# Optimization experiments

Measured on AMD Instinct MI355X. Metric: run time of the kernel, lower is better.

## Reference

```python
import jax, jax.numpy as jnp
import numpy as np

D_MODEL = 1024
D_STATE = 16
EPS = 1e-5


def _layernorm(x, g, b):
    mu = x.mean(-1, keepdims=True)
    xc = x - mu
    var = (xc * xc).mean(-1, keepdims=True)
    return xc * jax.lax.rsqrt(var + EPS) * g + b


def setup_inputs() -> dict:
    key = jax.random.key(0)
    ks = jax.random.split(key, 10)
    B, L, d, n = 8, 1024, D_MODEL, D_STATE
    s = 1.0 / np.sqrt(d)
    return {
        "x": jax.random.normal(ks[0], (B, L, d), jnp.float32),
        "h_prev": jnp.zeros((B, d * n), jnp.float32),
        "ln_g": jnp.ones((d,), jnp.float32),
        "ln_b": jnp.zeros((d,), jnp.float32),
        "W_ig": jax.random.uniform(ks[1], (2 * d, d), jnp.float32, -s, s),
        "W_dt": jax.random.uniform(ks[2], (d, d), jnp.float32, -s, s),
        "b_dt": jax.random.uniform(ks[3], (d,), jnp.float32, -s, s),
        "A_log": jax.random.uniform(ks[4], (d, n), jnp.float32, -3.0, -1.0),
        "W_B": jax.random.uniform(ks[5], (n, d), jnp.float32, -s, s),
        "W_C": jax.random.uniform(ks[6], (n, d), jnp.float32, -s, s),
        "D": jnp.ones((d,), jnp.float32),
        "W_out": jax.random.uniform(ks[7], (d, d), jnp.float32, -s, s),
    }


def reference(x, h_prev, ln_g, ln_b, W_ig, W_dt, b_dt, A_log, W_B, W_C, D, W_out):
    Bsz, L, d = x.shape
    n = A_log.shape[1]
    x_norm = _layernorm(x, ln_g, ln_b)
    x_proj = jnp.einsum('bld,ed->ble', x_norm, W_ig)  # [B,L,2d]
    x_in, z = x_proj[..., :d], x_proj[..., d:]
    dt = jax.nn.softplus(jnp.einsum('bld,ed->ble', x_in, W_dt) + b_dt)  # [B,L,d]
    A = -jnp.exp(A_log)  # [d,n]
    B_t = jnp.einsum('bld,nd->bln', x_in, W_B)  # [B,L,n]
    C_t = jnp.einsum('bld,nd->bln', x_in, W_C)  # [B,L,n]
    h0 = h_prev.reshape(Bsz, d, n)

    def step(h, inp):
        dt_t, xin_t, Bt_t, Ct_t = inp  # [B,d],[B,d],[B,n],[B,n]
        dA = jnp.exp(dt_t[..., None] * A)                      # [B,d,n]
        h = dA * h + (dt_t * xin_t)[..., None] * Bt_t[:, None, :]
        y_t = (h * Ct_t[:, None, :]).sum(-1)                   # [B,d]
        return h, y_t

    xs = (jnp.swapaxes(dt, 0, 1), jnp.swapaxes(x_in, 0, 1),
          jnp.swapaxes(B_t, 0, 1), jnp.swapaxes(C_t, 0, 1))
    h_final, y = jax.lax.scan(step, h0, xs)
    y = jnp.swapaxes(y, 0, 1)  # [B,L,d]
    ssm_out = y * jax.nn.silu(z) + x_in * D
    out = jnp.einsum('bld,ed->ble', ssm_out, W_out)
    return (x + out, h_final.reshape(Bsz, -1))
```

## Files before the change

kernel.cpp:

```cpp
#include <hip/hip_runtime.h>
#include <hip/hip_bf16.h>
#include <math.h>

#define DM 1024
#define NS 16
#define BSZ 8
#define LSEQ 1024
#define MROWS (BSZ*LSEQ)
#define CH 32
#define ROWP 36
#define YSP 18

typedef __bf16 bf16;
typedef bf16 bf16x8 __attribute__((ext_vector_type(8)));
typedef bf16 bf16x4 __attribute__((ext_vector_type(4)));
typedef float f32x4 __attribute__((ext_vector_type(4)));
typedef float f32x2 __attribute__((ext_vector_type(2)));
typedef unsigned int u32;
typedef unsigned short u16;
typedef u32 u32x4 __attribute__((ext_vector_type(4)));

__device__ __forceinline__ void async16(const void* g, void* l) {
  __builtin_amdgcn_global_load_lds((const __attribute__((address_space(1))) void*)g,
                                   (__attribute__((address_space(3))) void*)l,
                                   16, 0, 0);
}

__device__ __forceinline__ float bflo(u32 u) { return __builtin_bit_cast(float, (u32)(u << 16)); }
__device__ __forceinline__ float bfhi(u32 u) { return __builtin_bit_cast(float, (u32)(u & 0xffff0000u)); }

__global__ __launch_bounds__(256)
void preproc(const float* __restrict__ W_ig, const float* __restrict__ W_dt,
             const float* __restrict__ W_B, const float* __restrict__ W_C,
             const float* __restrict__ W_out,
             bf16* __restrict__ wmega, bf16* __restrict__ wstack,
             bf16* __restrict__ wout, bf16* __restrict__ wigT,
             const float* __restrict__ x, const float* __restrict__ ln_g,
             const float* __restrict__ ln_b, bf16* __restrict__ xnorm) {
  __shared__ float tile[64][65];
  const int blk = blockIdx.x;
  const int t = threadIdx.x;

  if (blk < 4128) {
    int i = blk * 256 + t;
    const float* s; bf16* d; int base;
    if (i < 524288)      { s = W_ig;  d = wmega;                           base = 0; }
    else if (i < 786432) { s = W_dt;  d = wstack;                          base = 524288; }
    else if (i < 790528) { s = W_B;   d = wstack + (size_t)DM * DM;        base = 786432; }
    else if (i < 794624) { s = W_C;   d = wstack + (size_t)(DM + NS) * DM; base = 790528; }
    else                 { s = W_out; d = wout;                            base = 794624; }
    int k = i - base;
    float4 v = ((const float4*)s)[k];
    bf16x4 o;
    o.x = (bf16)v.x; o.y = (bf16)v.y; o.z = (bf16)v.z; o.w = (bf16)v.w;
    *(bf16x4*)(d + 4 * (size_t)k) = o;
  } else if (blk < 4384) {
    int tb = blk - 4128;
    const int bk = (tb & 15) * 64;
    const int bd = (tb >> 4) * 64;
    const int c4 = t & 15;
    const int r0 = t >> 4;
#pragma unroll
    for (int p = 0; p < 4; ++p) {
      int r = r0 + p * 16;
      float4 v = *(const float4*)(W_ig + (size_t)(bd + r) * 1024 + bk + c4 * 4);
      tile[r][c4 * 4 + 0] = v.x;
      tile[r][c4 * 4 + 1] = v.y;
      tile[r][c4 * 4 + 2] = v.z;
      tile[r][c4 * 4 + 3] = v.w;
    }
    __syncthreads();
#pragma unroll
    for (int p = 0; p < 4; ++p) {
      int r = r0 + p * 16;
      bf16x4 o;
      o.x = (bf16)tile[c4 * 4 + 0][r];
      o.y = (bf16)tile[c4 * 4 + 1][r];
      o.z = (bf16)tile[c4 * 4 + 2][r];
      o.w = (bf16)tile[c4 * 4 + 3][r];
      *(bf16x4*)(wigT + (size_t)(bk + r) * 1024 + bd + c4 * 4) = o;
    }
  } else {
    const size_t row = blk - 4384;
    float4 v = ((const float4*)(x + row * DM))[t];
    float s = v.x + v.y + v.z + v.w;
    float s2 = v.x*v.x + v.y*v.y + v.z*v.z + v.w*v.w;
#pragma unroll
    for (int m = 1; m < 64; m <<= 1) { s += __shfl_xor(s, m, 64); s2 += __shfl_xor(s2, m, 64); }
    __shared__ float red[8];
    int wave = t >> 6, lane = t & 63;
    if (lane == 0) { red[wave] = s; red[4 + wave] = s2; }
    __syncthreads();
    s  = red[0] + red[1] + red[2] + red[3];
    s2 = red[4] + red[5] + red[6] + red[7];
    float mu  = s * (1.f / DM);
    float var = s2 * (1.f / DM) - mu * mu;
    float inv = rsqrtf(var + 1e-5f);
    float4 gg = ((const float4*)ln_g)[t];
    float4 bb = ((const float4*)ln_b)[t];
    bf16x4 o;
    o.x = (bf16)((v.x - mu) * inv * gg.x + bb.x);
    o.y = (bf16)((v.y - mu) * inv * gg.y + bb.y);
    o.z = (bf16)((v.z - mu) * inv * gg.z + bb.z);
    o.w = (bf16)((v.w - mu) * inv * gg.w + bb.w);
    *(bf16x4*)(xnorm + row * DM + t * 4) = o;
  }
}

template <int EPI, bool SWZ>
__global__ __launch_bounds__(256)
void gemm_bf16(const bf16* __restrict__ A, const bf16* __restrict__ W, int K,
               float* __restrict__ out_f, bf16* __restrict__ out_b,
               u16* __restrict__ out_u1, u16* __restrict__ out_u2,
               const float* __restrict__ aux,
               float* __restrict__ out_f3, float* __restrict__ out_f4) {
  __shared__ bf16 As[3][128 * 32];
  __shared__ bf16 Bs[3][128 * 32];
  int tx, ty;
  if (SWZ) {
    int g = blockIdx.x;
    int xcd = g & 7, slot = g >> 3;
    tx = slot >> 3;
    ty = xcd * 8 + (slot & 7);
  } else {
    tx = blockIdx.x; ty = blockIdx.y;
  }
  const int tid  = threadIdx.x;
  const int wave = tid >> 6, lane = tid & 63;
  const int lr = lane & 15, quad = lane >> 4;
  const size_t arow = (size_t)ty * 128;
  const size_t brow = (size_t)tx * 128;
  f32x4 acc[4][4] = {};

  const int srl  = lane >> 2;
  const int kg   = lane & 3;
  const int srow = wave * 32 + srl;
  const int skc  = (kg ^ ((srl >> 1) & 3)) * 8;
  const bf16* ag = A + (arow + srow) * (size_t)K + skc;
  const bf16* wg = W + (brow + srow) * (size_t)K + skc;

  const int soff = wave * 32 * 32;
  const int ra   = (((wave >> 1) * 64) + lr) * 32 + ((quad ^ ((lr >> 1) & 3)) * 8);
  const int rb   = (((wave & 1)  * 64) + lr) * 32 + ((quad ^ ((lr >> 1) & 3)) * 8);

  bf16 *aw0 = &As[0][soff], *aw1 = &As[1][soff], *aw2 = &As[2][soff];
  bf16 *bw0 = &Bs[0][soff], *bw1 = &Bs[1][soff], *bw2 = &Bs[2][soff];
  const bf16 *ar0 = &As[0][ra], *ar1 = &As[1][ra], *ar2 = &As[2][ra];
  const bf16 *br0 = &Bs[0][rb], *br1 = &Bs[1][rb], *br2 = &Bs[2][rb];

  auto STAGE = [&](bf16* adst, bf16* bdst, int kk) {
    async16(ag + kk,                       adst);
    async16(ag + (size_t)16 * K + kk,      adst + 16 * 32);
    async16(wg + kk,                       bdst);
    async16(wg + (size_t)16 * K + kk,      bdst + 16 * 32);
  };
  auto COMPUTE = [&](const bf16* ap, const bf16* bp) {
    bf16x8 af[4], bfr[4];
#pragma unroll
    for (int i = 0; i < 4; ++i) af[i] = *(const bf16x8*)(ap + i * 16 * 32);
#pragma unroll
    for (int j = 0; j < 4; ++j) bfr[j] = *(const bf16x8*)(bp + j * 16 * 32);
#pragma unroll
    for (int i = 0; i < 4; ++i)
#pragma unroll
      for (int j = 0; j < 4; ++j)
        acc[i][j] = __builtin_amdgcn_mfma_f32_16x16x32_bf16(af[i], bfr[j], acc[i][j], 0, 0, 0);
  };

  STAGE(aw0, bw0, 0);
  STAGE(aw1, bw1, 32);
  asm volatile("s_waitcnt vmcnt(4)" ::: "memory");
  __builtin_amdgcn_s_barrier();

  for (int k0 = 0; k0 < K; k0 += 32) {
    const bool pf = (k0 + 64 < K);
    if (pf) STAGE(aw2, bw2, k0 + 64);
    COMPUTE(ar0, br0);
    if (pf) asm volatile("s_waitcnt vmcnt(4)" ::: "memory");
    else    asm volatile("s_waitcnt vmcnt(0)" ::: "memory");
    __builtin_amdgcn_s_barrier();
    bf16* t0;
    t0 = aw0; aw0 = aw1; aw1 = aw2; aw2 = t0;
    t0 = bw0; bw0 = bw1; bw1 = bw2; bw2 = t0;
    const bf16* t1;
    t1 = ar0; ar0 = ar1; ar1 = ar2; ar2 = t1;
    t1 = br0; br0 = br1; br1 = br2; br2 = t1;
  }

  const size_t mbase = arow + (wave >> 1) * 64;
  const size_t nbase = brow + (wave & 1) * 64;
  if (EPI == 0) {
    if (nbase < 3 * DM) {
      u16* dst; size_t gbase; bool is_dt = false;
      if (nbase < DM)            { dst = out_u1;       gbase = nbase >> 4; }
      else if (nbase < 2 * DM)   { dst = (u16*)out_b;  gbase = (nbase - DM) >> 4; }
      else                       { dst = out_u2;       gbase = (nbase - 2 * DM) >> 4; is_dt = true; }
      bf16* lds_ep = &As[0][0] + (size_t)wave * 1024;
#pragma unroll
      for (int j = 0; j < 4; ++j) {
#pragma unroll
        for (int i = 0; i < 4; ++i)
#pragma unroll
          for (int r = 0; r < 4; ++r) {
            float v = acc[i][j][r];
            if (is_dt) {
              float tt = v + aux[nbase - 2 * DM + j * 16 + lr];
              v = (tt > 20.f) ? tt : __logf(1.f + __expf(tt));
            }
            lds_ep[(i * 16 + quad * 4 + r) * 16 + lr] = (bf16)v;
          }
        u32x4 v0 = *(u32x4*)&lds_ep[lane * 16];
        u32x4 v1 = *(u32x4*)&lds_ep[lane * 16 + 8];
        size_t off = ((gbase + j) * (size_t)MROWS + mbase + lane) * 16;
        *(u32x4*)&dst[off]     = v0;
        *(u32x4*)&dst[off + 8] = v1;
      }
    } else if (nbase < 3 * DM + 2 * NS) {
#pragma unroll
      for (int i = 0; i < 4; ++i)
#pragma unroll
        for (int r = 0; r < 4; ++r) {
          size_t m = mbase + i * 16 + quad * 4 + r;
          out_f3[m * NS + lr] = acc[i][0][r];
          out_f4[m * NS + lr] = acc[i][1][r];
        }
    }
  } else {
#pragma unroll
    for (int i = 0; i < 4; ++i)
#pragma unroll
      for (int j = 0; j < 4; ++j)
#pragma unroll
        for (int r = 0; r < 4; ++r) {
          size_t m = mbase + i * 16 + quad * 4 + r;
          size_t n = nbase + j * 16 + lr;
          float v = acc[i][j][r];
          if (EPI == 2) {
            out_f[m * DM + n] = v + aux[m * DM + n];
          } else {
            out_b[m * (size_t)DM + n] = (bf16)v;
          }
        }
  }
}

__global__ __launch_bounds__(256)
void scan_kernel(const u16* __restrict__ dt_b, const u16* __restrict__ xi_b,
                 const bf16* __restrict__ z_b,
                 const float* __restrict__ B_t, const float* __restrict__ C_t,
                 const float* __restrict__ A_log, const float* __restrict__ h_prev,
                 const float* __restrict__ Dvec,
                 bf16* __restrict__ ssm_out, float* __restrict__ h_final) {
  const int blk = blockIdx.x;
  const int b = blk >> 6;
  const int g = blk & 63;
  const int d0 = g * 16;
  const int t = threadIdx.x;
  const int n = t & 15, dl = t >> 4;
  const int d = d0 + dl;
  const float Ac2 = -__expf(A_log[d * NS + n]) * 1.44269504f;
  float h = h_prev[(size_t)b * DM * NS + (size_t)d * NS + n];

  __shared__ u32   dxs[2][16][ROWP];
  __shared__ float Bsh[2][16][ROWP];
  __shared__ float Csh[2][16][ROWP];
  __shared__ float ys_p[CH][16][YSP];

  const size_t base_row = (size_t)b * LSEQ;
  const size_t base16 = ((size_t)g * MROWS + base_row) * 16;
  const int pl = t >> 3, pc = (2 * t) & 15;
  const int l_a = t >> 4, c_a = t & 15;
  const float Dva = Dvec[d0 + c_a];

  {
    u32 D = ((const u32*)(dt_b + base16))[t];
    u32 X = ((const u32*)(xi_b + base16))[t];
    dxs[0][pc][pl]     = (D & 0xffffu) | (X << 16);
    dxs[0][pc + 1][pl] = (D >> 16) | (X & 0xffff0000u);
    size_t gB = base_row * NS;
    f32x2 B2 = ((const f32x2*)(B_t + gB))[t];
    f32x2 C2 = ((const f32x2*)(C_t + gB))[t];
    Bsh[0][pc][pl] = B2.x;  Bsh[0][pc + 1][pl] = B2.y;
    Csh[0][pc][pl] = C2.x;  Csh[0][pc + 1][pl] = C2.y;
  }
  float za = (float)z_b[base16 + t];
  float zb = (float)z_b[base16 + 256 + t];
  __syncthreads();

  for (int c = 0; c < LSEQ / CH; ++c) {
    const int cur = c & 1, nxt = cur ^ 1;
    u32 pD, pX; f32x2 pB2, pC2; float pza, pzb;
    if (c + 1 < LSEQ / CH) {
      size_t off = base16 + (size_t)(c + 1) * (CH * 16);
      pD = ((const u32*)(dt_b + off))[t];
      pX = ((const u32*)(xi_b + off))[t];
      pza = (float)z_b[off + t]; pzb = (float)z_b[off + 256 + t];
      size_t gB = (base_row + (size_t)(c + 1) * CH) * NS;
      pB2 = ((const f32x2*)(B_t + gB))[t];
      pC2 = ((const f32x2*)(C_t + gB))[t];
    }
#pragma unroll
    for (int l4 = 0; l4 < CH; l4 += 4) {
      u32x4 dx4 = *(const u32x4*)&dxs[cur][dl][l4];
      f32x4 b4  = *(const f32x4*)&Bsh[cur][n][l4];
      f32x4 c4  = *(const f32x4*)&Csh[cur][n][l4];
#pragma unroll
      for (int i = 0; i < 4; ++i) {
        float dtv = bflo(dx4[i]), xiv = bfhi(dx4[i]);
        float a = __builtin_amdgcn_exp2f(dtv * Ac2);
        h = fmaf(a, h, (dtv * xiv) * b4[i]);
        ys_p[l4 + i][dl][n] = h * c4[i];
      }
    }
    __syncthreads();
    {
      const f32x2* r1 = (const f32x2*)&ys_p[l_a][c_a][0];
      const f32x2* r2 = (const f32x2*)&ys_p[l_a + 16][c_a][0];
      float s1 = 0.f, s2 = 0.f;
#pragma unroll
      for (int k = 0; k < 8; ++k) {
        f32x2 v1 = r1[k], v2 = r2[k];
        s1 += v1.x + v1.y;
        s2 += v2.x + v2.y;
      }
      float x1 = bfhi(dxs[cur][c_a][l_a]);
      float x2 = bfhi(dxs[cur][c_a][l_a + 16]);
      float g1 = za / (1.f + __expf(-za));
      float g2 = zb / (1.f + __expf(-zb));
      size_t l0 = (size_t)c * CH;
      ssm_out[(base_row + l0 + l_a) * DM + d0 + c_a]      = (bf16)(s1 * g1 + x1 * Dva);
      ssm_out[(base_row + l0 + l_a + 16) * DM + d0 + c_a] = (bf16)(s2 * g2 + x2 * Dva);
    }
    if (c + 1 < LSEQ / CH) {
      dxs[nxt][pc][pl]     = (pD & 0xffffu) | (pX << 16);
      dxs[nxt][pc + 1][pl] = (pD >> 16) | (pX & 0xffff0000u);
      Bsh[nxt][pc][pl] = pB2.x;  Bsh[nxt][pc + 1][pl] = pB2.y;
      Csh[nxt][pc][pl] = pC2.x;  Csh[nxt][pc + 1][pl] = pC2.y;
      za = pza; zb = pzb;
    }
    __syncthreads();
  }
  h_final[(size_t)b * DM * NS + (size_t)d0 * NS + t] = h;
}

extern "C" void kernel_launch(void* const* d_in, const int* in_sizes, int n_in,
                              void* d_out, int out_size, void* d_ws, size_t ws_size,
                              hipStream_t stream) {
  const float* x      = (const float*)d_in[0];
  const float* h_prev = (const float*)d_in[1];
  const float* ln_g   = (const float*)d_in[2];
  const float* ln_b   = (const float*)d_in[3];
  const float* W_ig   = (const float*)d_in[4];
  const float* W_dt   = (const float*)d_in[5];
  const float* b_dt   = (const float*)d_in[6];
  const float* A_log  = (const float*)d_in[7];
  const float* W_B    = (const float*)d_in[8];
  const float* W_C    = (const float*)d_in[9];
  const float* Dvec   = (const float*)d_in[10];
  const float* W_out  = (const float*)d_in[11];

  char* ws = (char*)d_ws;
  size_t off = 0;
  auto alloc = [&](size_t bytes) -> char* {
    char* p = ws + off;
    off += (bytes + 255) & ~(size_t)255;
    return p;
  };
  bf16*  wmega_b = (bf16*)alloc((size_t)3200 * DM * 2);
  bf16*  wstack_b= (bf16*)alloc((size_t)1152 * DM * 2);
  bf16*  wigT_b  = (bf16*)alloc((size_t)DM * DM * 2);
  bf16*  wout_b  = (bf16*)alloc((size_t)DM * DM * 2);
  bf16*  xnorm_b = (bf16*)alloc((size_t)MROWS * DM * 2);
  u16*   xi_w    = (u16*)alloc((size_t)MROWS * DM * 2);
  u16*   dt_w    = (u16*)alloc((size_t)MROWS * DM * 2);
  bf16*  z_bb    = (bf16*)alloc((size_t)MROWS * DM * 2);
  bf16*  ssm_b   = (bf16*)alloc((size_t)MROWS * DM * 2);
  float* Bt      = (float*)alloc((size_t)MROWS * NS * 4);
  float* Ct      = (float*)alloc((size_t)MROWS * NS * 4);
  (void)ws_size; (void)in_sizes; (void)n_in; (void)out_size;

  float* out_main = (float*)d_out;
  float* out_h    = (float*)d_out + (size_t)MROWS * DM;

  preproc<<<12576, 256, 0, stream>>>(W_ig, W_dt, W_B, W_C, W_out,
                                     wmega_b, wstack_b, wout_b, wigT_b,
                                     x, ln_g, ln_b, xnorm_b);

  gemm_bf16<3, false><<<dim3(8, 9), 256, 0, stream>>>(wstack_b, wigT_b, DM,
      nullptr, wmega_b + (size_t)2048 * DM, nullptr, nullptr, nullptr, nullptr, nullptr);

  gemm_bf16<0, true><<<1600, 256, 0, stream>>>(xnorm_b, wmega_b, DM,
      nullptr, z_bb, xi_w, dt_w, b_dt, Bt, Ct);

  scan_kernel<<<512, 256, 0, stream>>>(dt_w, xi_w, z_bb, Bt, Ct, A_log, h_prev,
                                       Dvec, ssm_b, out_h);

  gemm_bf16<2, true><<<512, 256, 0, stream>>>(ssm_b, wout_b, DM,
      out_main, nullptr, nullptr, nullptr, x, nullptr, nullptr);
}
```

Baseline: 309.7 us.

## Replace mega input GEMM with 256x256-tile 512-thread kernel and padded weights

Adds a dedicated 256x256-tile GEMM kernel with 512 threads, XOR-swizzled LDS, double buffering and staggered async loads interleaved with MFMA groups for the fused x_in/z/dt/B/C projection. The weight matrix is padded to 3328 rows and zero-filled in preproc so the N dimension divides the tile. The aim is more data reuse per tile and fewer blocks than the 128x128 version. The cost is padded wasted compute on the B/C tail and heavier register and LDS use per block, which can limit occupancy.

```diff
diff --git a/kernel.cpp b/kernel.cpp
--- a/kernel.cpp
+++ b/kernel.cpp
@@ -10,6 +10,7 @@
 #define CH 32
 #define ROWP 36
 #define YSP 18
+#define NPAD 3328
 
 typedef __bf16 bf16;
 typedef bf16 bf16x8 __attribute__((ext_vector_type(8)));
@@ -80,7 +81,7 @@
       o.w = (bf16)tile[c4 * 4 + 3][r];
       *(bf16x4*)(wigT + (size_t)(bk + r) * 1024 + bd + c4 * 4) = o;
     }
-  } else {
+  } else if (blk < 12576) {
     const size_t row = blk - 4384;
     float4 v = ((const float4*)(x + row * DM))[t];
     float s = v.x + v.y + v.z + v.w;
@@ -104,16 +105,178 @@
     o.z = (bf16)((v.z - mu) * inv * gg.z + bb.z);
     o.w = (bf16)((v.w - mu) * inv * gg.w + bb.w);
     *(bf16x4*)(xnorm + row * DM + t * 4) = o;
-  }
+  } else {
+    size_t idx = (size_t)(blk - 12576) * 256 + t;
+    bf16x8 z = {};
+    *(bf16x8*)(wmega + (size_t)3200 * DM + idx * 8) = z;
+  }
+}
+
+__global__ __launch_bounds__(512, 2)
+void gemm256_mega(const bf16* __restrict__ A, const bf16* __restrict__ W,
+                  bf16* __restrict__ out_z, u16* __restrict__ out_xi,
+                  u16* __restrict__ out_dt, const float* __restrict__ aux,
+                  float* __restrict__ out_B, float* __restrict__ out_C) {
+  __shared__ bf16 As2[2][256 * 64];
+  __shared__ bf16 Bs2[2][256 * 64];
+  const int K = 1024;
+
+  const int g = blockIdx.x;
+  const int xcd = g & 7, local = g >> 3;
+  const int tx = local >> 2;
+  const int ty = xcd * 4 + (local & 3);
+
+  const int tid = threadIdx.x;
+  const int w = tid >> 6, lane = tid & 63;
+  const int wm = w >> 2, wn = w & 3;
+  const int lr = lane & 15, quad = lane >> 4;
+  const int swz = (lr >> 1) & 7;
+  const size_t arow = (size_t)ty * 256;
+  const size_t brow = (size_t)tx * 256;
+
+  f32x4 acc[8][4] = {};
+
+  const bf16 *asrc0, *asrc1, *asrc2, *asrc3, *wsrc0, *wsrc1, *wsrc2, *wsrc3;
+  {
+#define SRC_INIT(s) {                                                   \
+    int chunk = w * 64 + lane + (s) * 512;                              \
+    int row = chunk >> 3;                                               \
+    int logical = (chunk & 7) ^ ((row >> 1) & 7);                       \
+    asrc##s = A + (arow + row) * (size_t)K + logical * 8;               \
+    wsrc##s = W + (brow + row) * (size_t)K + logical * 8; }
+    SRC_INIT(0) SRC_INIT(1) SRC_INIT(2) SRC_INIT(3)
+#undef SRC_INIT
+  }
+
+#define STAGE256(buf, s, koff)                                           \
+  do {                                                                   \
+    async16(asrc##s + (koff), &As2[buf][0] + ((s) * 512 + w * 64) * 8);  \
+    async16(wsrc##s + (koff), &Bs2[buf][0] + ((s) * 512 + w * 64) * 8);  \
+  } while (0)
+
+#define RD_A(bufp, mh, af)                                               \
+  _Pragma("unroll")                                                      \
+  for (int i = 0; i < 4; ++i) {                                          \
+    _Pragma("unroll")                                                    \
+    for (int s = 0; s < 2; ++s)                                          \
+      af[i][s] = *(const bf16x8*)((bufp) +                               \
+        (wm * 128 + ((mh) * 4 + i) * 16 + lr) * 64 +                     \
+        ((s * 4 + quad) ^ swz) * 8);                                     \
+  }
+#define RD_B(bufp, bfr)                                                  \
+  _Pragma("unroll")                                                      \
+  for (int j = 0; j < 4; ++j) {                                          \
+    _Pragma("unroll")                                                    \
+    for (int s = 0; s < 2; ++s)                                          \
+      bfr[j][s] = *(const bf16x8*)((bufp) +                              \
+        (wn * 64 + j * 16 + lr) * 64 +                                   \
+        ((s * 4 + quad) ^ swz) * 8);                                     \
+  }
+#define MMQ(af, bfr, mh, nh)                                             \
+  do {                                                                   \
+    __builtin_amdgcn_s_setprio(1);                                       \
+    _Pragma("unroll")                                                    \
+    for (int i = 0; i < 4; ++i)                                          \
+      _Pragma("unroll")                                                  \
+      for (int jj = 0; jj < 2; ++jj)                                     \
+        _Pragma("unroll")                                                \
+        for (int s = 0; s < 2; ++s)                                      \
+          acc[(mh) * 4 + i][(nh) * 2 + jj] =                             \
+            __builtin_amdgcn_mfma_f32_16x16x32_bf16(                     \
+              af[i][s], bfr[(nh) * 2 + jj][s],                           \
+              acc[(mh) * 4 + i][(nh) * 2 + jj], 0, 0, 0);                \
+    __builtin_amdgcn_s_setprio(0);                                       \
+  } while (0)
+
+  STAGE256(0, 0, 0); STAGE256(0, 1, 0); STAGE256(0, 2, 0); STAGE256(0, 3, 0);
+  asm volatile("s_waitcnt vmcnt(0)" ::: "memory");
+  __builtin_amdgcn_s_barrier();
+
+  for (int kt = 0; kt < 16; ++kt) {
+    const int buf = kt & 1, nbuf = buf ^ 1;
+    const int koff = (kt + 1) * 64;
+    const bf16* Ab = buf ? &As2[1][0] : &As2[0][0];
+    const bf16* Bb = buf ? &Bs2[1][0] : &Bs2[0][0];
+    const bool pf = (kt < 15);
+    bf16x8 af[4][2], bfr[4][2];
+
+    RD_A(Ab, 0, af)
+    RD_B(Bb, bfr)
+    if (pf) { if (nbuf) { STAGE256(1, 0, koff); STAGE256(1, 1, koff); }
+              else      { STAGE256(0, 0, koff); STAGE256(0, 1, koff); } }
+    __builtin_amdgcn_s_barrier();
+    MMQ(af, bfr, 0, 0);
+    __builtin_amdgcn_s_barrier();
+
+    if (pf) { if (nbuf) STAGE256(1, 2, koff); else STAGE256(0, 2, koff); }
+    __builtin_amdgcn_s_barrier();
+    MMQ(af, bfr, 0, 1);
+    __builtin_amdgcn_s_barrier();
+
+    RD_A(Ab, 1, af)
+    if (pf) { if (nbuf) STAGE256(1, 3, koff); else STAGE256(0, 3, koff); }
+    __builtin_amdgcn_s_barrier();
+    MMQ(af, bfr, 1, 1);
+    __builtin_amdgcn_s_barrier();
+
+    asm volatile("s_waitcnt vmcnt(0)" ::: "memory");
+    __builtin_amdgcn_s_barrier();
+    MMQ(af, bfr, 1, 0);
+    __builtin_amdgcn_s_barrier();
+  }
+
+  const size_t mb = arow + (size_t)wm * 128;
+  const size_t nb = brow + (size_t)wn * 64;
+  if (nb < 3 * DM) {
+    u16* dst; size_t gbase; bool is_dt = false;
+    if (nb < DM)          { dst = out_xi;      gbase = nb >> 4; }
+    else if (nb < 2 * DM) { dst = (u16*)out_z; gbase = (nb - DM) >> 4; }
+    else                  { dst = out_dt;      gbase = (nb - 2 * DM) >> 4; is_dt = true; }
+    bf16* lds_ep = &As2[0][0] + (size_t)w * 2048;
+#pragma unroll
+    for (int j = 0; j < 4; ++j) {
+#pragma unroll
+      for (int i = 0; i < 8; ++i)
+#pragma unroll
+        for (int r = 0; r < 4; ++r) {
+          float v = acc[i][j][r];
+          if (is_dt) {
+            float tt = v + aux[nb - 2 * DM + j * 16 + lr];
+            v = (tt > 20.f) ? tt : __logf(1.f + __expf(tt));
+          }
+          lds_ep[(i * 16 + quad * 4 + r) * 16 + lr] = (bf16)v;
+        }
+#pragma unroll
+      for (int rr = 0; rr < 2; ++rr) {
+        int row = rr * 64 + lane;
+        u32x4 v0 = *(u32x4*)&lds_ep[row * 16];
+        u32x4 v1 = *(u32x4*)&lds_ep[row * 16 + 8];
+        size_t off = ((gbase + j) * (size_t)MROWS + mb + row) * 16;
+        *(u32x4*)&dst[off]     = v0;
+        *(u32x4*)&dst[off + 8] = v1;
+      }
+    }
+  } else if (nb < 3 * DM + 2 * NS) {
+#pragma unroll
+    for (int i = 0; i < 8; ++i)
+#pragma unroll
+      for (int r = 0; r < 4; ++r) {
+        size_t m = mb + i * 16 + quad * 4 + r;
+        out_B[m * NS + lr] = acc[i][0][r];
+        out_C[m * NS + lr] = acc[i][1][r];
+      }
+  }
+#undef STAGE256
+#undef RD_A
+#undef RD_B
+#undef MMQ
 }
 
 template <int EPI, bool SWZ>
 __global__ __launch_bounds__(256)
 void gemm_bf16(const bf16* __restrict__ A, const bf16* __restrict__ W, int K,
                float* __restrict__ out_f, bf16* __restrict__ out_b,
-               u16* __restrict__ out_u1, u16* __restrict__ out_u2,
-               const float* __restrict__ aux,
-               float* __restrict__ out_f3, float* __restrict__ out_f4) {
+               const float* __restrict__ aux) {
   __shared__ bf16 As[3][128 * 32];
   __shared__ bf16 Bs[3][128 * 32];
   int tx, ty;
@@ -189,59 +352,21 @@
 
   const size_t mbase = arow + (wave >> 1) * 64;
   const size_t nbase = brow + (wave & 1) * 64;
-  if (EPI == 0) {
-    if (nbase < 3 * DM) {
-      u16* dst; size_t gbase; bool is_dt = false;
-      if (nbase < DM)            { dst = out_u1;       gbase = nbase >> 4; }
-      else if (nbase < 2 * DM)   { dst = (u16*)out_b;  gbase = (nbase - DM) >> 4; }
-      else                       { dst = out_u2;       gbase = (nbase - 2 * DM) >> 4; is_dt = true; }
-      bf16* lds_ep = &As[0][0] + (size_t)wave * 1024;
-#pragma unroll
-      for (int j = 0; j < 4; ++j) {
-#pragma unroll
-        for (int i = 0; i < 4; ++i)
-#pragma unroll
-          for (int r = 0; r < 4; ++r) {
-            float v = acc[i][j][r];
-            if (is_dt) {
-              float tt = v + aux[nbase - 2 * DM + j * 16 + lr];
-              v = (tt > 20.f) ? tt : __logf(1.f + __expf(tt));
-            }
-            lds_ep[(i * 16 + quad * 4 + r) * 16 + lr] = (bf16)v;
-          }
-        u32x4 v0 = *(u32x4*)&lds_ep[lane * 16];
-        u32x4 v1 = *(u32x4*)&lds_ep[lane * 16 + 8];
-        size_t off = ((gbase + j) * (size_t)MROWS + mbase + lane) * 16;
-        *(u32x4*)&dst[off]     = v0;
-        *(u32x4*)&dst[off + 8] = v1;
+#pragma unroll
+  for (int i = 0; i < 4; ++i)
+#pragma unroll
+    for (int j = 0; j < 4; ++j)
+#pragma unroll
+      for (int r = 0; r < 4; ++r) {
+        size_t m = mbase + i * 16 + quad * 4 + r;
+        size_t n = nbase + j * 16 + lr;
+        float v = acc[i][j][r];
+        if (EPI == 2) {
+          out_f[m * DM + n] = v + aux[m * DM + n];
+        } else {
+          out_b[m * (size_t)DM + n] = (bf16)v;
+        }
       }
-    } else if (nbase < 3 * DM + 2 * NS) {
-#pragma unroll
-      for (int i = 0; i < 4; ++i)
-#pragma unroll
-        for (int r = 0; r < 4; ++r) {
-          size_t m = mbase + i * 16 + quad * 4 + r;
-          out_f3[m * NS + lr] = acc[i][0][r];
-          out_f4[m * NS + lr] = acc[i][1][r];
-        }
-    }
-  } else {
-#pragma unroll
-    for (int i = 0; i < 4; ++i)
-#pragma unroll
-      for (int j = 0; j < 4; ++j)
-#pragma unroll
-        for (int r = 0; r < 4; ++r) {
-          size_t m = mbase + i * 16 + quad * 4 + r;
-          size_t n = nbase + j * 16 + lr;
-          float v = acc[i][j][r];
-          if (EPI == 2) {
-            out_f[m * DM + n] = v + aux[m * DM + n];
-          } else {
-            out_b[m * (size_t)DM + n] = (bf16)v;
-          }
-        }
-  }
 }
 
 __global__ __launch_bounds__(256)
@@ -366,7 +491,7 @@
     off += (bytes + 255) & ~(size_t)255;
     return p;
   };
-  bf16*  wmega_b = (bf16*)alloc((size_t)3200 * DM * 2);
+  bf16*  wmega_b = (bf16*)alloc((size_t)NPAD * DM * 2);
   bf16*  wstack_b= (bf16*)alloc((size_t)1152 * DM * 2);
   bf16*  wigT_b  = (bf16*)alloc((size_t)DM * DM * 2);
   bf16*  wout_b  = (bf16*)alloc((size_t)DM * DM * 2);
@@ -382,19 +507,19 @@
   float* out_main = (float*)d_out;
   float* out_h    = (float*)d_out + (size_t)MROWS * DM;
 
-  preproc<<<12576, 256, 0, stream>>>(W_ig, W_dt, W_B, W_C, W_out,
+  preproc<<<12640, 256, 0, stream>>>(W_ig, W_dt, W_B, W_C, W_out,
                                      wmega_b, wstack_b, wout_b, wigT_b,
                                      x, ln_g, ln_b, xnorm_b);
 
   gemm_bf16<3, false><<<dim3(8, 9), 256, 0, stream>>>(wstack_b, wigT_b, DM,
-      nullptr, wmega_b + (size_t)2048 * DM, nullptr, nullptr, nullptr, nullptr, nullptr);
-
-  gemm_bf16<0, true><<<1600, 256, 0, stream>>>(xnorm_b, wmega_b, DM,
-      nullptr, z_bb, xi_w, dt_w, b_dt, Bt, Ct);
+      nullptr, wmega_b + (size_t)2048 * DM, nullptr);
+
+  gemm256_mega<<<416, 512, 0, stream>>>(xnorm_b, wmega_b,
+      z_bb, xi_w, dt_w, b_dt, Bt, Ct);
 
   scan_kernel<<<512, 256, 0, stream>>>(dt_w, xi_w, z_bb, Bt, Ct, A_log, h_prev,
                                        Dvec, ssm_b, out_h);
 
   gemm_bf16<2, true><<<512, 256, 0, stream>>>(ssm_b, wout_b, DM,
-      out_main, nullptr, nullptr, nullptr, x, nullptr, nullptr);
+      out_main, nullptr, x);
 }
```

Result: no change. 314.2 us (+1.5%).
